# Kernel optimization log

Hardware: AMD Instinct MI355X
Metric: run time of the kernel (lower is better)

## Reference

```python
import jax, jax.numpy as jnp
import numpy as np

B, N, CS, CZ, H, C, PQ, PV = 1, 512, 384, 128, 12, 16, 4, 8
INF, EPS = 1e5, 1e-8


def _quat_to_rot(q):
    # q: [..., 4] unit quaternion -> [..., 3, 3] rotation matrix
    w, x, y, z = q[..., 0], q[..., 1], q[..., 2], q[..., 3]
    r0 = jnp.stack([1 - 2 * (y * y + z * z), 2 * (x * y - w * z), 2 * (x * z + w * y)], -1)
    r1 = jnp.stack([2 * (x * y + w * z), 1 - 2 * (x * x + z * z), 2 * (y * z - w * x)], -1)
    r2 = jnp.stack([2 * (x * z - w * y), 2 * (y * z + w * x), 1 - 2 * (x * x + y * y)], -1)
    return jnp.stack([r0, r1, r2], -2)


def setup_inputs() -> dict:
    key = jax.random.key(0)
    ks = jax.random.split(key, 20)
    sc = 0.02
    quat = jax.random.normal(ks[0], (B, N, 4), jnp.float32)
    quat = quat / jnp.linalg.norm(quat, axis=-1, keepdims=True)
    concat_dim = H * (C + PV * 4 + CZ)
    return {
        "s": jax.random.normal(ks[1], (B, N, CS), jnp.float32),
        "z": jax.random.normal(ks[2], (B, N, N, CZ), jnp.float32),
        "rot": _quat_to_rot(quat),
        "trans": jax.random.normal(ks[3], (B, N, 3), jnp.float32),
        "mask": jnp.ones((B, N), jnp.float32),
        "W_q": jax.random.normal(ks[4], (CS, H * C), jnp.float32) * sc,
        "b_q": jnp.zeros((H * C,), jnp.float32),
        "W_kv": jax.random.normal(ks[5], (CS, 2 * H * C), jnp.float32) * sc,
        "b_kv": jnp.zeros((2 * H * C,), jnp.float32),
        "W_qp": jax.random.normal(ks[6], (CS, H * PQ * 3), jnp.float32) * sc,
        "b_qp": jnp.zeros((H * PQ * 3,), jnp.float32),
        "W_kvp": jax.random.normal(ks[7], (CS, H * (PQ + PV) * 3), jnp.float32) * sc,
        "b_kvp": jnp.zeros((H * (PQ + PV) * 3,), jnp.float32),
        "W_b": jax.random.normal(ks[8], (CZ, H), jnp.float32) * sc,
        "b_b": jnp.zeros((H,), jnp.float32),
        "head_weights": jnp.full((H,), 0.541324854612918, jnp.float32),  # softplus^-1(1)
        "W_out": jax.random.normal(ks[9], (concat_dim, CS), jnp.float32) * sc,
        "b_out": jnp.zeros((CS,), jnp.float32),
    }


def reference(s, z, rot, trans, mask, W_q, b_q, W_kv, b_kv, W_qp, b_qp, W_kvp, b_kvp,
              W_b, b_b, head_weights, W_out, b_out):
    # scalar projections
    q = (s @ W_q + b_q).reshape(*s.shape[:-1], H, C)              # [B,N,H,C]
    kv = (s @ W_kv + b_kv).reshape(*s.shape[:-1], H, 2 * C)
    k, v = kv[..., :C], kv[..., C:]                               # [B,N,H,C]

    def to_global_pts(lin, npts):
        # lin: [B,N,H*npts*3]; torch layout: split into thirds -> stack as xyz
        p = jnp.stack(jnp.split(lin, 3, axis=-1), axis=-1)        # [B,N,H*npts,3]
        g = jnp.einsum('bnij,bnpj->bnpi', rot, p) + trans[:, :, None, :]
        return g.reshape(*g.shape[:-2], H, npts, 3)

    q_pts = to_global_pts(s @ W_qp + b_qp, PQ)                    # [B,N,H,PQ,3]
    kv_pts = to_global_pts(s @ W_kvp + b_kvp, PQ + PV)
    k_pts, v_pts = kv_pts[..., :PQ, :], kv_pts[..., PQ:, :]       # [B,N,H,PQ/PV,3]

    # attention logits
    bias = z @ W_b + b_b                                          # [B,N,N,H]
    a = jnp.einsum('bihc,bjhc->bhij', q, k) * np.sqrt(1.0 / (3 * C))
    a = a + np.sqrt(1.0 / 3.0) * jnp.transpose(bias, (0, 3, 1, 2))

    d = q_pts[:, :, None] - k_pts[:, None]                        # [B,N,N,H,PQ,3]
    pt_att = jnp.sum(d * d, axis=-1)                              # [B,N,N,H,PQ]
    hw = jax.nn.softplus(head_weights) * np.sqrt(1.0 / (3 * (PQ * 9.0 / 2)))
    pt_att = jnp.sum(pt_att * hw[None, None, None, :, None], axis=-1) * (-0.5)  # [B,N,N,H]
    a = a + jnp.transpose(pt_att, (0, 3, 1, 2))

    sq_mask = INF * (mask[:, :, None] * mask[:, None, :] - 1.0)   # [B,N,N]
    a = jax.nn.softmax(a + sq_mask[:, None], axis=-1)             # [B,H,N,N]

    # aggregation
    o = jnp.einsum('bhij,bjhc->bihc', a, v).reshape(*s.shape[:-1], H * C)
    o_pt = jnp.einsum('bhij,bjhpc->bihpc', a, v_pts)              # [B,N,H,PV,3]
    o_pt = jnp.einsum('bnji,bnhpj->bnhpi', rot, o_pt - trans[:, :, None, None, :])
    o_pt_norm = jnp.sqrt(jnp.sum(o_pt ** 2, -1) + EPS).reshape(*s.shape[:-1], H * PV)
    o_pt = o_pt.reshape(*s.shape[:-1], H * PV, 3)
    o_pair = jnp.einsum('bhij,bijc->bihc', a, z).reshape(*s.shape[:-1], H * CZ)

    cat = jnp.concatenate([o, o_pt[..., 0], o_pt[..., 1], o_pt[..., 2], o_pt_norm, o_pair], -1)
    return cat @ W_out + b_out                                    # [B,N,CS]
```

## Files before the change

### kernel.cpp

```cpp
#include <hip/hip_runtime.h>
#include <hip/hip_bf16.h>
#include <math.h>


#define N_    512
#define CS_   384
#define CZ_   128
#define H_    12
#define INF_  100000.0f
#define EPS_  1e-8f

__global__ __launch_bounds__(256) void proj_gemm(
    const float* __restrict__ A,
    const float* __restrict__ W0, const float* __restrict__ b0, float* __restrict__ C0, int N0,
    const float* __restrict__ W1, const float* __restrict__ b1, float* __restrict__ C1, int N1,
    const float* __restrict__ W2, const float* __restrict__ b2, float* __restrict__ C2, int N2,
    const float* __restrict__ W3, const float* __restrict__ b3, float* __restrict__ C3, int N3)
{
    const float* W; const float* bias; float* C; int Nt;
    switch (blockIdx.z) {
        case 0:  W = W0; bias = b0; C = C0; Nt = N0; break;
        case 1:  W = W1; bias = b1; C = C1; Nt = N1; break;
        case 2:  W = W2; bias = b2; C = C2; Nt = N2; break;
        default: W = W3; bias = b3; C = C3; Nt = N3; break;
    }
    const int n0 = blockIdx.y * 64;
    if (n0 >= Nt) return;
    const int m0 = blockIdx.x * 64;

    __shared__ float As[16 * 68];
    __shared__ float Bs[16 * 68];
    const int t  = threadIdx.x;
    const int tm = t & 15;
    const int tn = t >> 4;

    float acc[4][4];
    #pragma unroll
    for (int r = 0; r < 4; ++r)
        #pragma unroll
        for (int c = 0; c < 4; ++c) acc[r][c] = 0.f;

    for (int k0 = 0; k0 < CS_; k0 += 16) {
        {
            int m = t >> 2, kb = (t & 3) * 4;
            float4 a4 = *(const float4*)(A + (size_t)(m0 + m) * CS_ + k0 + kb);
            As[(kb + 0) * 68 + m] = a4.x;
            As[(kb + 1) * 68 + m] = a4.y;
            As[(kb + 2) * 68 + m] = a4.z;
            As[(kb + 3) * 68 + m] = a4.w;
        }
        {
            int kk = t >> 4, n = (t & 15) * 4;
            int gn = n0 + n;
            const float* wr = W + (size_t)(k0 + kk) * Nt;
            float4 b4;
            b4.x = (gn + 0 < Nt) ? wr[gn + 0] : 0.f;
            b4.y = (gn + 1 < Nt) ? wr[gn + 1] : 0.f;
            b4.z = (gn + 2 < Nt) ? wr[gn + 2] : 0.f;
            b4.w = (gn + 3 < Nt) ? wr[gn + 3] : 0.f;
            *(float4*)(Bs + kk * 68 + n) = b4;
        }
        __syncthreads();
        #pragma unroll
        for (int kk = 0; kk < 16; ++kk) {
            float4 a4 = *(const float4*)(As + kk * 68 + tm * 4);
            float4 b4 = *(const float4*)(Bs + kk * 68 + tn * 4);
            float am[4] = {a4.x, a4.y, a4.z, a4.w};
            float bn[4] = {b4.x, b4.y, b4.z, b4.w};
            #pragma unroll
            for (int r = 0; r < 4; ++r)
                #pragma unroll
                for (int c = 0; c < 4; ++c)
                    acc[r][c] = fmaf(am[r], bn[c], acc[r][c]);
        }
        __syncthreads();
    }
    #pragma unroll
    for (int r = 0; r < 4; ++r) {
        int gm = m0 + tm * 4 + r;
        int gn = n0 + tn * 4;
        float* cr = C + (size_t)gm * Nt;
        #pragma unroll
        for (int c = 0; c < 4; ++c)
            if (gn + c < Nt) cr[gn + c] = acc[r][c] + bias[gn + c];
    }
}

__global__ __launch_bounds__(256) void gemm_ksplit(
    const float* __restrict__ A, const float* __restrict__ W,
    float* __restrict__ P)
{
    const int kc = blockIdx.z;
    const int m0 = blockIdx.x * 64;
    const int n0 = blockIdx.y * 64;

    __shared__ float As[16 * 68];
    __shared__ float Bs[16 * 68];
    const int t  = threadIdx.x;
    const int tm = t & 15;
    const int tn = t >> 4;

    float acc[4][4];
    #pragma unroll
    for (int r = 0; r < 4; ++r)
        #pragma unroll
        for (int c = 0; c < 4; ++c) acc[r][c] = 0.f;

    const int kbeg = kc * 192;
    for (int k0 = kbeg; k0 < kbeg + 192; k0 += 16) {
        {
            int m = t >> 2, kb = (t & 3) * 4;
            float4 a4 = *(const float4*)(A + (size_t)(m0 + m) * 2112 + k0 + kb);
            As[(kb + 0) * 68 + m] = a4.x;
            As[(kb + 1) * 68 + m] = a4.y;
            As[(kb + 2) * 68 + m] = a4.z;
            As[(kb + 3) * 68 + m] = a4.w;
        }
        {
            int kk = t >> 4, n = (t & 15) * 4;
            float4 b4 = *(const float4*)(W + (size_t)(k0 + kk) * 384 + n0 + n);
            *(float4*)(Bs + kk * 68 + n) = b4;
        }
        __syncthreads();
        #pragma unroll
        for (int kk = 0; kk < 16; ++kk) {
            float4 a4 = *(const float4*)(As + kk * 68 + tm * 4);
            float4 b4 = *(const float4*)(Bs + kk * 68 + tn * 4);
            float am[4] = {a4.x, a4.y, a4.z, a4.w};
            float bn[4] = {b4.x, b4.y, b4.z, b4.w};
            #pragma unroll
            for (int r = 0; r < 4; ++r)
                #pragma unroll
                for (int c = 0; c < 4; ++c)
                    acc[r][c] = fmaf(am[r], bn[c], acc[r][c]);
        }
        __syncthreads();
    }
    float* Pk = P + (size_t)kc * (512 * 384);
    #pragma unroll
    for (int r = 0; r < 4; ++r) {
        int gm = m0 + tm * 4 + r;
        *(float4*)(Pk + (size_t)gm * 384 + n0 + tn * 4) =
            make_float4(acc[r][0], acc[r][1], acc[r][2], acc[r][3]);
    }
}

__global__ __launch_bounds__(256) void reduce_out(
    const float* __restrict__ P, const float* __restrict__ bias,
    float* __restrict__ out)
{
    int idx = blockIdx.x * 256 + threadIdx.x;
    const float4* b4 = (const float4*)bias;
    float4 s = b4[idx % 96];
    const float4* P4 = (const float4*)P;
    #pragma unroll
    for (int g = 0; g < 11; ++g) {
        float4 v = P4[(size_t)g * 49152 + idx];
        s.x += v.x; s.y += v.y; s.z += v.z; s.w += v.w;
    }
    ((float4*)out)[idx] = s;
}

__global__ __launch_bounds__(192) void prep_points(
    const float* __restrict__ lqp, const float* __restrict__ lkvp,
    const float* __restrict__ rot, const float* __restrict__ trans,
    const float* __restrict__ kvb,
    float* __restrict__ qp, float* __restrict__ kp,
    float* __restrict__ vcat)
{
    const int n = blockIdx.x;
    const int t = threadIdx.x;
    const float* R = rot   + n * 9;
    const float* T = trans + n * 3;

    if (t < 48) {
        float p0 = lqp[n * 144 + t];
        float p1 = lqp[n * 144 + 48 + t];
        float p2 = lqp[n * 144 + 96 + t];
        float* d = qp + n * 144 + t * 3;
        d[0] = R[0]*p0 + R[1]*p1 + R[2]*p2 + T[0];
        d[1] = R[3]*p0 + R[4]*p1 + R[5]*p2 + T[1];
        d[2] = R[6]*p0 + R[7]*p1 + R[8]*p2 + T[2];
    } else {
        int jj = t - 48;
        float p0 = lkvp[n * 432 + jj];
        float p1 = lkvp[n * 432 + 144 + jj];
        float p2 = lkvp[n * 432 + 288 + jj];
        float g0 = R[0]*p0 + R[1]*p1 + R[2]*p2 + T[0];
        float g1 = R[3]*p0 + R[4]*p1 + R[5]*p2 + T[1];
        float g2 = R[6]*p0 + R[7]*p1 + R[8]*p2 + T[2];
        int h = jj / 12, idx = jj % 12;
        if (idx < 4) {
            float* d = kp + n * 144 + (h * 4 + idx) * 3;
            d[0] = g0; d[1] = g1; d[2] = g2;
        } else {
            float* d = vcat + (size_t)n * 512 + 192 + h * 24 + (idx - 4) * 3;
            d[0] = g0; d[1] = g1; d[2] = g2;
        }
    }
    vcat[(size_t)n * 512 + t] = kvb[(size_t)n * 384 + (t >> 4) * 32 + 16 + (t & 15)];
}

__global__ __launch_bounds__(256) void ipa_core(
    const float* __restrict__ z,   const float* __restrict__ q,
    const float* __restrict__ kvb, const float* __restrict__ qp,
    const float* __restrict__ kp,  const float* __restrict__ vcat,
    const float* __restrict__ Wb,  const float* __restrict__ bb,
    const float* __restrict__ hwraw, const float* __restrict__ mask,
    const float* __restrict__ rot, const float* __restrict__ trans,
    float* __restrict__ cat)
{
    __shared__ float4 a_s4[1548];
    __shared__ float4 pb4[2112];
    float* a_s = (float*)a_s4;
    float* pb  = (float*)pb4;

    const int i    = blockIdx.x;
    const int t    = threadIdx.x;
    const int lane = t & 63;

    const float sc_qk = 0.14433756729740643f;
    const float sc_b  = 0.5773502691896258f;
    const float sc_hw = 0.13608276348795434f;

    const float mi = mask[i];

    const int h0 = __builtin_amdgcn_readfirstlane((t >> 6) * 3);
    const float bbA = bb[h0],     bbB = bb[h0 + 1],     bbC = bb[h0 + 2];
    float xA = hwraw[h0], xB = hwraw[h0 + 1], xC = hwraw[h0 + 2];
    const float hwA = ((xA > 20.f) ? xA : log1pf(__expf(xA))) * sc_hw;
    const float hwB = ((xB > 20.f) ? xB : log1pf(__expf(xB))) * sc_hw;
    const float hwC = ((xC > 20.f) ? xC : log1pf(__expf(xC))) * sc_hw;

    const float4* qv  = (const float4*)(q  + (size_t)i * 192);
    const float4* qpv = (const float4*)(qp + (size_t)i * 144);

    float* ztile = pb;
    for (int tile = 0; tile < 8; ++tile) {
        const int jb = tile * 64;
        const float4* zsrc = (const float4*)z + ((size_t)i * N_ + jb) * 32;
        #pragma unroll
        for (int k2 = 0; k2 < 8; ++k2) {
            int idx = t + k2 * 256;
            int rr = idx >> 5, c4 = idx & 31;
            *(float4*)(ztile + rr * 132 + c4 * 4) = zsrc[(size_t)rr * 32 + c4];
        }
        __syncthreads();

        const int j = jb + lane;
        float b0 = bbA, b1 = bbB, b2 = bbC;
        const float4* zrow = (const float4*)(ztile + lane * 132);
        #pragma unroll 8
        for (int c4 = 0; c4 < 32; ++c4) {
            float4 z4 = zrow[c4];
            float zc[4] = {z4.x, z4.y, z4.z, z4.w};
            #pragma unroll
            for (int cc = 0; cc < 4; ++cc) {
                const int c = c4 * 4 + cc;
                b0 = fmaf(zc[cc], Wb[c * 12 + h0    ], b0);
                b1 = fmaf(zc[cc], Wb[c * 12 + h0 + 1], b1);
                b2 = fmaf(zc[cc], Wb[c * 12 + h0 + 2], b2);
            }
        }

        const float mt = INF_ * (mi * mask[j] - 1.f);
        const float4* kr  = (const float4*)(kvb + (size_t)j * 384);
        const float4* kpr = (const float4*)(kp  + (size_t)j * 144);
        #pragma unroll
        for (int hh = 0; hh < 3; ++hh) {
            const int h = h0 + hh;
            float qk = 0.f;
            #pragma unroll
            for (int c4 = 0; c4 < 4; ++c4) {
                float4 qh = qv[h * 4 + c4];
                float4 kh = kr[h * 8 + c4];
                qk = fmaf(qh.x, kh.x, qk);
                qk = fmaf(qh.y, kh.y, qk);
                qk = fmaf(qh.z, kh.z, qk);
                qk = fmaf(qh.w, kh.w, qk);
            }
            float pt = 0.f;
            #pragma unroll
            for (int r = 0; r < 3; ++r) {
                float4 qh = qpv[h * 3 + r];
                float4 kh = kpr[h * 3 + r];
                float d0 = qh.x - kh.x, d1 = qh.y - kh.y;
                float d2 = qh.z - kh.z, d3 = qh.w - kh.w;
                pt = fmaf(d0, d0, pt); pt = fmaf(d1, d1, pt);
                pt = fmaf(d2, d2, pt); pt = fmaf(d3, d3, pt);
            }
            float bsum = (hh == 0) ? b0 : (hh == 1) ? b1 : b2;
            float hwv  = (hh == 0) ? hwA : (hh == 1) ? hwB : hwC;
            a_s[h * 516 + j] = fmaf(qk, sc_qk,
                               fmaf(bsum, sc_b,
                               fmaf(-0.5f * hwv, pt, mt)));
        }
        __syncthreads();
    }

    {
        const int w = t >> 6;
        #pragma unroll
        for (int hh = 0; hh < 3; ++hh) {
            const int h = w + hh * 4;
            float* row = a_s + h * 516;
            float4 v0 = *(float4*)(row + lane * 8);
            float4 v1 = *(float4*)(row + lane * 8 + 4);
            float m = fmaxf(fmaxf(fmaxf(v0.x, v0.y), fmaxf(v0.z, v0.w)),
                            fmaxf(fmaxf(v1.x, v1.y), fmaxf(v1.z, v1.w)));
            #pragma unroll
            for (int off = 32; off > 0; off >>= 1)
                m = fmaxf(m, __shfl_xor(m, off));
            v0.x = __expf(v0.x - m); v0.y = __expf(v0.y - m);
            v0.z = __expf(v0.z - m); v0.w = __expf(v0.w - m);
            v1.x = __expf(v1.x - m); v1.y = __expf(v1.y - m);
            v1.z = __expf(v1.z - m); v1.w = __expf(v1.w - m);
            float s = v0.x + v0.y + v0.z + v0.w + v1.x + v1.y + v1.z + v1.w;
            #pragma unroll
            for (int off = 32; off > 0; off >>= 1)
                s += __shfl_xor(s, off);
            float inv = 1.f / s;
            v0.x *= inv; v0.y *= inv; v0.z *= inv; v0.w *= inv;
            v1.x *= inv; v1.y *= inv; v1.z *= inv; v1.w *= inv;
            *(float4*)(row + lane * 8)     = v0;
            *(float4*)(row + lane * 8 + 4) = v1;
        }
    }
    __syncthreads();

    float* opt_s = pb;
    if (t < 240) {
        const int o0 = 2 * t;
        const int h  = (o0 < 192) ? (o0 >> 4) : ((o0 - 192) / 24);
        const float2* vrow = (const float2*)vcat + t;
        float accx = 0.f, accy = 0.f;
        #pragma unroll 4
        for (int j = 0; j < 512; ++j) {
            float2 v2 = vrow[(size_t)j * 256];
            float aj  = a_s[h * 516 + j];
            accx = fmaf(aj, v2.x, accx);
            accy = fmaf(aj, v2.y, accy);
        }
        if (o0 < 192) {
            cat[(size_t)i * 2112 + o0]     = accx;
            cat[(size_t)i * 2112 + o0 + 1] = accy;
        } else {
            opt_s[o0 - 192] = accx;
            opt_s[o0 - 191] = accy;
        }
    }
    __syncthreads();

    if (t < 96) {
        const float* R = rot   + i * 9;
        const float* T = trans + i * 3;
        float g0 = opt_s[t * 3 + 0] - T[0];
        float g1 = opt_s[t * 3 + 1] - T[1];
        float g2 = opt_s[t * 3 + 2] - T[2];
        float x  = R[0]*g0 + R[3]*g1 + R[6]*g2;
        float y  = R[1]*g0 + R[4]*g1 + R[7]*g2;
        float zz = R[2]*g0 + R[5]*g1 + R[8]*g2;
        float nrm = sqrtf(x*x + y*y + zz*zz + EPS_);
        float* cr = cat + (size_t)i * 2112;
        cr[192 + t] = x;
        cr[288 + t] = y;
        cr[384 + t] = zz;
        cr[480 + t] = nrm;
    }
    __syncthreads();

    {
        const int c4 = t & 31;
        const int jg = t >> 5;
        float4 acc[12];
        #pragma unroll
        for (int h = 0; h < 12; ++h) acc[h] = make_float4(0.f, 0.f, 0.f, 0.f);

        const float4* zr = (const float4*)z + (size_t)i * (N_ * 32) + c4;
        for (int j4b = 0; j4b < 16; ++j4b) {
            const int jb = jg * 64 + j4b * 4;
            float4 zv[4];
            #pragma unroll
            for (int u = 0; u < 4; ++u) zv[u] = zr[(size_t)(jb + u) * 32];
            #pragma unroll
            for (int h = 0; h < 12; ++h) {
                float4 a4 = *(const float4*)(a_s + h * 516 + jb);
                acc[h].x = fmaf(a4.x, zv[0].x, acc[h].x);
                acc[h].y = fmaf(a4.x, zv[0].y, acc[h].y);
                acc[h].z = fmaf(a4.x, zv[0].z, acc[h].z);
                acc[h].w = fmaf(a4.x, zv[0].w, acc[h].w);
                acc[h].x = fmaf(a4.y, zv[1].x, acc[h].x);
                acc[h].y = fmaf(a4.y, zv[1].y, acc[h].y);
                acc[h].z = fmaf(a4.y, zv[1].z, acc[h].z);
                acc[h].w = fmaf(a4.y, zv[1].w, acc[h].w);
                acc[h].x = fmaf(a4.z, zv[2].x, acc[h].x);
                acc[h].y = fmaf(a4.z, zv[2].y, acc[h].y);
                acc[h].z = fmaf(a4.z, zv[2].z, acc[h].z);
                acc[h].w = fmaf(a4.z, zv[2].w, acc[h].w);
                acc[h].x = fmaf(a4.w, zv[3].x, acc[h].x);
                acc[h].y = fmaf(a4.w, zv[3].y, acc[h].y);
                acc[h].z = fmaf(a4.w, zv[3].z, acc[h].z);
                acc[h].w = fmaf(a4.w, zv[3].w, acc[h].w);
            }
        }

        #pragma unroll
        for (int half = 0; half < 2; ++half) {
            __syncthreads();
            #pragma unroll
            for (int hh = 0; hh < 6; ++hh)
                *(float4*)(pb + (size_t)(jg * 6 + hh) * 132 + c4 * 4) = acc[half * 6 + hh];
            __syncthreads();
            #pragma unroll
            for (int k = 0; k < 3; ++k) {
                const int idx = t + k * 256;
                const int hh = idx >> 7, c = idx & 127;
                float s = 0.f;
                #pragma unroll
                for (int g = 0; g < 8; ++g)
                    s += pb[(size_t)(g * 6 + hh) * 132 + c];
                cat[(size_t)i * 2112 + 576 + half * 768 + idx] = s;
            }
        }
    }
}

extern "C" void kernel_launch(void* const* d_in, const int* in_sizes, int n_in,
                              void* d_out, int out_size, void* d_ws, size_t ws_size,
                              hipStream_t stream)
{
    const float* s     = (const float*)d_in[0];
    const float* z     = (const float*)d_in[1];
    const float* rot   = (const float*)d_in[2];
    const float* trans = (const float*)d_in[3];
    const float* mask  = (const float*)d_in[4];
    const float* W_q   = (const float*)d_in[5];
    const float* b_q   = (const float*)d_in[6];
    const float* W_kv  = (const float*)d_in[7];
    const float* b_kv  = (const float*)d_in[8];
    const float* W_qp  = (const float*)d_in[9];
    const float* b_qp  = (const float*)d_in[10];
    const float* W_kvp = (const float*)d_in[11];
    const float* b_kvp = (const float*)d_in[12];
    const float* W_b   = (const float*)d_in[13];
    const float* b_b   = (const float*)d_in[14];
    const float* hw    = (const float*)d_in[15];
    const float* W_out = (const float*)d_in[16];
    const float* b_out = (const float*)d_in[17];
    float* out = (float*)d_out;
    float* ws  = (float*)d_ws;

    float* gpart = ws;
    float* cat   = ws + 2162688;
    float* q     = ws;
    float* kvb   = q    + 98304;
    float* lqp   = kvb  + 196608;
    float* lkvp  = lqp  + 73728;
    float* qp    = lkvp + 221184;
    float* kp    = qp   + 73728;
    float* vcat  = kp   + 73728;

    proj_gemm<<<dim3(8, 7, 4), 256, 0, stream>>>(
        s,
        W_q,   b_q,   q,    192,
        W_kv,  b_kv,  kvb,  384,
        W_qp,  b_qp,  lqp,  144,
        W_kvp, b_kvp, lkvp, 432);
    prep_points<<<512, 192, 0, stream>>>(lqp, lkvp, rot, trans, kvb, qp, kp, vcat);
    ipa_core<<<512, 256, 0, stream>>>(z, q, kvb, qp, kp, vcat,
                                      W_b, b_b, hw, mask, rot, trans, cat);
    gemm_ksplit<<<dim3(8, 6, 11), 256, 0, stream>>>(cat, W_out, gpart);
    reduce_out<<<192, 256, 0, stream>>>(gpart, b_out, out);
}
```

Measured before the change: 387.5 us.

## Split monolithic IPA kernel into GEMM-based logits, bias, softmax and pair-aggregation kernels

The single per-row ipa_core kernel becomes four kernels. qkpt_gemm expands the point-distance term algebraically (|q|^2 + |k|^2 - 2q·k) so the QK and point logits become one tiled GEMM over a concatenated 28-wide feature. logits_k adds the pair bias from z, smax_av does softmax and value aggregation, and opair_k does the z-weighted pair aggregation. The goal is more parallelism and tiled reuse than one 512-block kernel gives. The cost is materialising a 12x512x512 attention tensor in global memory and reading z twice across kernels.

Result: faster. 374.2 us (-3.4%).

```diff
diff --git a/kernel.cpp b/kernel.cpp
--- a/kernel.cpp
+++ b/kernel.cpp
@@ -5,10 +5,16 @@
 
 #define N_    512
 #define CS_   384
-#define CZ_   128
-#define H_    12
 #define INF_  100000.0f
 #define EPS_  1e-8f
+
+#define SC_QK 0.14433756729740643f
+#define SC_B  0.5773502691896258f
+#define SC_HW 0.13608276348795434f
+
+__device__ __forceinline__ float softplus_(float x) {
+    return (x > 20.f) ? x : log1pf(__expf(x));
+}
 
 __global__ __launch_bounds__(256) void proj_gemm(
     const float* __restrict__ A,
@@ -86,87 +92,14 @@
     }
 }
 
-__global__ __launch_bounds__(256) void gemm_ksplit(
-    const float* __restrict__ A, const float* __restrict__ W,
-    float* __restrict__ P)
-{
-    const int kc = blockIdx.z;
-    const int m0 = blockIdx.x * 64;
-    const int n0 = blockIdx.y * 64;
-
-    __shared__ float As[16 * 68];
-    __shared__ float Bs[16 * 68];
-    const int t  = threadIdx.x;
-    const int tm = t & 15;
-    const int tn = t >> 4;
-
-    float acc[4][4];
-    #pragma unroll
-    for (int r = 0; r < 4; ++r)
-        #pragma unroll
-        for (int c = 0; c < 4; ++c) acc[r][c] = 0.f;
-
-    const int kbeg = kc * 192;
-    for (int k0 = kbeg; k0 < kbeg + 192; k0 += 16) {
-        {
-            int m = t >> 2, kb = (t & 3) * 4;
-            float4 a4 = *(const float4*)(A + (size_t)(m0 + m) * 2112 + k0 + kb);
-            As[(kb + 0) * 68 + m] = a4.x;
-            As[(kb + 1) * 68 + m] = a4.y;
-            As[(kb + 2) * 68 + m] = a4.z;
-            As[(kb + 3) * 68 + m] = a4.w;
-        }
-        {
-            int kk = t >> 4, n = (t & 15) * 4;
-            float4 b4 = *(const float4*)(W + (size_t)(k0 + kk) * 384 + n0 + n);
-            *(float4*)(Bs + kk * 68 + n) = b4;
-        }
-        __syncthreads();
-        #pragma unroll
-        for (int kk = 0; kk < 16; ++kk) {
-            float4 a4 = *(const float4*)(As + kk * 68 + tm * 4);
-            float4 b4 = *(const float4*)(Bs + kk * 68 + tn * 4);
-            float am[4] = {a4.x, a4.y, a4.z, a4.w};
-            float bn[4] = {b4.x, b4.y, b4.z, b4.w};
-            #pragma unroll
-            for (int r = 0; r < 4; ++r)
-                #pragma unroll
-                for (int c = 0; c < 4; ++c)
-                    acc[r][c] = fmaf(am[r], bn[c], acc[r][c]);
-        }
-        __syncthreads();
-    }
-    float* Pk = P + (size_t)kc * (512 * 384);
-    #pragma unroll
-    for (int r = 0; r < 4; ++r) {
-        int gm = m0 + tm * 4 + r;
-        *(float4*)(Pk + (size_t)gm * 384 + n0 + tn * 4) =
-            make_float4(acc[r][0], acc[r][1], acc[r][2], acc[r][3]);
-    }
-}
-
-__global__ __launch_bounds__(256) void reduce_out(
-    const float* __restrict__ P, const float* __restrict__ bias,
-    float* __restrict__ out)
-{
-    int idx = blockIdx.x * 256 + threadIdx.x;
-    const float4* b4 = (const float4*)bias;
-    float4 s = b4[idx % 96];
-    const float4* P4 = (const float4*)P;
-    #pragma unroll
-    for (int g = 0; g < 11; ++g) {
-        float4 v = P4[(size_t)g * 49152 + idx];
-        s.x += v.x; s.y += v.y; s.z += v.z; s.w += v.w;
-    }
-    ((float4*)out)[idx] = s;
-}
-
 __global__ __launch_bounds__(192) void prep_points(
     const float* __restrict__ lqp, const float* __restrict__ lkvp,
     const float* __restrict__ rot, const float* __restrict__ trans,
-    const float* __restrict__ kvb,
+    const float* __restrict__ kvb, const float* __restrict__ q,
+    const float* __restrict__ hwraw,
     float* __restrict__ qp, float* __restrict__ kp,
-    float* __restrict__ vcat)
+    float* __restrict__ vcat, float* __restrict__ qcat,
+    float* __restrict__ kcat, float* __restrict__ qn, float* __restrict__ kn)
 {
     const int n = blockIdx.x;
     const int t = threadIdx.x;
@@ -199,110 +132,169 @@
         }
     }
     vcat[(size_t)n * 512 + t] = kvb[(size_t)n * 384 + (t >> 4) * 32 + 16 + (t & 15)];
-}
-
-__global__ __launch_bounds__(256) void ipa_core(
-    const float* __restrict__ z,   const float* __restrict__ q,
-    const float* __restrict__ kvb, const float* __restrict__ qp,
-    const float* __restrict__ kp,  const float* __restrict__ vcat,
-    const float* __restrict__ Wb,  const float* __restrict__ bb,
-    const float* __restrict__ hwraw, const float* __restrict__ mask,
+    __syncthreads();
+
+    {
+        int h = t >> 4, c = t & 15;
+        qcat[((size_t)h * 512 + n) * 28 + c] = q[(size_t)n * 192 + t];
+        kcat[((size_t)h * 512 + n) * 28 + c] = kvb[(size_t)n * 384 + h * 32 + c] * SC_QK;
+    }
+    if (t < 144) {
+        int h = t / 12;
+        float hw = softplus_(hwraw[h]) * SC_HW;
+        qcat[((size_t)h * 512 + n) * 28 + 16 + (t - h * 12)] = qp[n * 144 + t];
+        kcat[((size_t)h * 512 + n) * 28 + 16 + (t - h * 12)] = kp[n * 144 + t] * hw;
+    }
+    if (t < 24) {
+        int h = t % 12;
+        float hw = softplus_(hwraw[h]) * SC_HW;
+        const float* src = (t < 12) ? (qp + n * 144 + h * 12) : (kp + n * 144 + h * 12);
+        float s = 0.f;
+        #pragma unroll
+        for (int r = 0; r < 12; ++r) { float v = src[r]; s = fmaf(v, v, s); }
+        float* dst = (t < 12) ? qn : kn;
+        dst[h * 512 + n] = 0.5f * hw * s;
+    }
+}
+
+__global__ __launch_bounds__(256) void qkpt_gemm(
+    const float* __restrict__ qcat, const float* __restrict__ kcat,
+    const float* __restrict__ qn,   const float* __restrict__ kn,
+    const float* __restrict__ mask, float* __restrict__ att)
+{
+    const int jt = blockIdx.x, it = blockIdx.y, h = blockIdx.z;
+    __shared__ float As[28 * 68];
+    __shared__ float Bs[28 * 68];
+    __shared__ float qn_s[64], kn_s[64], mI[64], mJ[64];
+
+    const int t  = threadIdx.x;
+    const int tm = t & 15;
+    const int tn = t >> 4;
+
+    const float* Aq = qcat + ((size_t)h * 512 + it * 64) * 28;
+    const float* Bk = kcat + ((size_t)h * 512 + jt * 64) * 28;
+    for (int idx = t; idx < 448; idx += 256) {
+        int row = idx / 7, c4 = idx % 7;
+        float4 a4 = *(const float4*)(Aq + row * 28 + c4 * 4);
+        As[(c4 * 4 + 0) * 68 + row] = a4.x;
+        As[(c4 * 4 + 1) * 68 + row] = a4.y;
+        As[(c4 * 4 + 2) * 68 + row] = a4.z;
+        As[(c4 * 4 + 3) * 68 + row] = a4.w;
+        float4 b4 = *(const float4*)(Bk + row * 28 + c4 * 4);
+        Bs[(c4 * 4 + 0) * 68 + row] = b4.x;
+        Bs[(c4 * 4 + 1) * 68 + row] = b4.y;
+        Bs[(c4 * 4 + 2) * 68 + row] = b4.z;
+        Bs[(c4 * 4 + 3) * 68 + row] = b4.w;
+    }
+    if (t < 64) {
+        qn_s[t] = qn[h * 512 + it * 64 + t];
+        mI[t]   = mask[it * 64 + t];
+    } else if (t < 128) {
+        kn_s[t - 64] = kn[h * 512 + jt * 64 + (t - 64)];
+        mJ[t - 64]   = mask[jt * 64 + (t - 64)];
+    }
+    __syncthreads();
+
+    float acc[4][4];
+    #pragma unroll
+    for (int r = 0; r < 4; ++r)
+        #pragma unroll
+        for (int c = 0; c < 4; ++c) acc[r][c] = 0.f;
+
+    #pragma unroll
+    for (int kk = 0; kk < 28; ++kk) {
+        float4 a4 = *(const float4*)(As + kk * 68 + tm * 4);
+        float4 b4 = *(const float4*)(Bs + kk * 68 + tn * 4);
+        float am[4] = {a4.x, a4.y, a4.z, a4.w};
+        float bn[4] = {b4.x, b4.y, b4.z, b4.w};
+        #pragma unroll
+        for (int r = 0; r < 4; ++r)
+            #pragma unroll
+            for (int c = 0; c < 4; ++c)
+                acc[r][c] = fmaf(am[r], bn[c], acc[r][c]);
+    }
+
+    #pragma unroll
+    for (int r = 0; r < 4; ++r) {
+        const int i_ = it * 64 + tm * 4 + r;
+        float* dst = att + ((size_t)h * 512 + i_) * 512 + jt * 64 + tn * 4;
+        float4 o;
+        float qnr = qn_s[tm * 4 + r], mir = mI[tm * 4 + r];
+        o.x = acc[r][0] - qnr - kn_s[tn*4+0] + INF_ * (mir * mJ[tn*4+0] - 1.f);
+        o.y = acc[r][1] - qnr - kn_s[tn*4+1] + INF_ * (mir * mJ[tn*4+1] - 1.f);
+        o.z = acc[r][2] - qnr - kn_s[tn*4+2] + INF_ * (mir * mJ[tn*4+2] - 1.f);
+        o.w = acc[r][3] - qnr - kn_s[tn*4+3] + INF_ * (mir * mJ[tn*4+3] - 1.f);
+        *(float4*)dst = o;
+    }
+}
+
+__global__ __launch_bounds__(256) void logits_k(
+    const float* __restrict__ z, const float* __restrict__ Wb,
+    const float* __restrict__ bb, float* __restrict__ att)
+{
+    __shared__ float ztile[64 * 132];
+    const int jt   = blockIdx.x;
+    const int i    = blockIdx.y;
+    const int jb   = jt * 64;
+    const int t    = threadIdx.x;
+    const int lane = t & 63;
+
+    const int h0 = __builtin_amdgcn_readfirstlane((t >> 6) * 3);
+    const float bbA = bb[h0], bbB = bb[h0 + 1], bbC = bb[h0 + 2];
+
+    const float4* zsrc = (const float4*)z + ((size_t)i * N_ + jb) * 32;
+    #pragma unroll
+    for (int k2 = 0; k2 < 8; ++k2) {
+        int idx = t + k2 * 256;
+        int rr = idx >> 5, c4 = idx & 31;
+        *(float4*)(ztile + rr * 132 + c4 * 4) = zsrc[(size_t)rr * 32 + c4];
+    }
+    __syncthreads();
+
+    float b0 = bbA, b1 = bbB, b2 = bbC;
+    const float4* zrow = (const float4*)(ztile + lane * 132);
+    #pragma unroll 8
+    for (int c4 = 0; c4 < 32; ++c4) {
+        float4 z4 = zrow[c4];
+        float zc[4] = {z4.x, z4.y, z4.z, z4.w};
+        #pragma unroll
+        for (int cc = 0; cc < 4; ++cc) {
+            const int c = c4 * 4 + cc;
+            b0 = fmaf(zc[cc], Wb[c * 12 + h0    ], b0);
+            b1 = fmaf(zc[cc], Wb[c * 12 + h0 + 1], b1);
+            b2 = fmaf(zc[cc], Wb[c * 12 + h0 + 2], b2);
+        }
+    }
+
+    const size_t base = ((size_t)h0 * 512 + i) * 512 + jb + lane;
+    att[base]              = fmaf(SC_B, b0, att[base]);
+    att[base + 262144]     = fmaf(SC_B, b1, att[base + 262144]);
+    att[base + 2 * 262144] = fmaf(SC_B, b2, att[base + 2 * 262144]);
+}
+
+__global__ __launch_bounds__(384) void smax_av(
+    float* __restrict__ att, const float* __restrict__ vcat,
     const float* __restrict__ rot, const float* __restrict__ trans,
     float* __restrict__ cat)
 {
-    __shared__ float4 a_s4[1548];
-    __shared__ float4 pb4[2112];
-    float* a_s = (float*)a_s4;
-    float* pb  = (float*)pb4;
-
+    __shared__ float a_s[12 * 516];
+    __shared__ float opt_s[288];
     const int i    = blockIdx.x;
     const int t    = threadIdx.x;
     const int lane = t & 63;
 
-    const float sc_qk = 0.14433756729740643f;
-    const float sc_b  = 0.5773502691896258f;
-    const float sc_hw = 0.13608276348795434f;
-
-    const float mi = mask[i];
-
-    const int h0 = __builtin_amdgcn_readfirstlane((t >> 6) * 3);
-    const float bbA = bb[h0],     bbB = bb[h0 + 1],     bbC = bb[h0 + 2];
-    float xA = hwraw[h0], xB = hwraw[h0 + 1], xC = hwraw[h0 + 2];
-    const float hwA = ((xA > 20.f) ? xA : log1pf(__expf(xA))) * sc_hw;
-    const float hwB = ((xB > 20.f) ? xB : log1pf(__expf(xB))) * sc_hw;
-    const float hwC = ((xC > 20.f) ? xC : log1pf(__expf(xC))) * sc_hw;
-
-    const float4* qv  = (const float4*)(q  + (size_t)i * 192);
-    const float4* qpv = (const float4*)(qp + (size_t)i * 144);
-
-    float* ztile = pb;
-    for (int tile = 0; tile < 8; ++tile) {
-        const int jb = tile * 64;
-        const float4* zsrc = (const float4*)z + ((size_t)i * N_ + jb) * 32;
-        #pragma unroll
-        for (int k2 = 0; k2 < 8; ++k2) {
-            int idx = t + k2 * 256;
-            int rr = idx >> 5, c4 = idx & 31;
-            *(float4*)(ztile + rr * 132 + c4 * 4) = zsrc[(size_t)rr * 32 + c4];
-        }
-        __syncthreads();
-
-        const int j = jb + lane;
-        float b0 = bbA, b1 = bbB, b2 = bbC;
-        const float4* zrow = (const float4*)(ztile + lane * 132);
-        #pragma unroll 8
-        for (int c4 = 0; c4 < 32; ++c4) {
-            float4 z4 = zrow[c4];
-            float zc[4] = {z4.x, z4.y, z4.z, z4.w};
-            #pragma unroll
-            for (int cc = 0; cc < 4; ++cc) {
-                const int c = c4 * 4 + cc;
-                b0 = fmaf(zc[cc], Wb[c * 12 + h0    ], b0);
-                b1 = fmaf(zc[cc], Wb[c * 12 + h0 + 1], b1);
-                b2 = fmaf(zc[cc], Wb[c * 12 + h0 + 2], b2);
-            }
-        }
-
-        const float mt = INF_ * (mi * mask[j] - 1.f);
-        const float4* kr  = (const float4*)(kvb + (size_t)j * 384);
-        const float4* kpr = (const float4*)(kp  + (size_t)j * 144);
-        #pragma unroll
-        for (int hh = 0; hh < 3; ++hh) {
-            const int h = h0 + hh;
-            float qk = 0.f;
-            #pragma unroll
-            for (int c4 = 0; c4 < 4; ++c4) {
-                float4 qh = qv[h * 4 + c4];
-                float4 kh = kr[h * 8 + c4];
-                qk = fmaf(qh.x, kh.x, qk);
-                qk = fmaf(qh.y, kh.y, qk);
-                qk = fmaf(qh.z, kh.z, qk);
-                qk = fmaf(qh.w, kh.w, qk);
-            }
-            float pt = 0.f;
-            #pragma unroll
-            for (int r = 0; r < 3; ++r) {
-                float4 qh = qpv[h * 3 + r];
-                float4 kh = kpr[h * 3 + r];
-                float d0 = qh.x - kh.x, d1 = qh.y - kh.y;
-                float d2 = qh.z - kh.z, d3 = qh.w - kh.w;
-                pt = fmaf(d0, d0, pt); pt = fmaf(d1, d1, pt);
-                pt = fmaf(d2, d2, pt); pt = fmaf(d3, d3, pt);
-            }
-            float bsum = (hh == 0) ? b0 : (hh == 1) ? b1 : b2;
-            float hwv  = (hh == 0) ? hwA : (hh == 1) ? hwB : hwC;
-            a_s[h * 516 + j] = fmaf(qk, sc_qk,
-                               fmaf(bsum, sc_b,
-                               fmaf(-0.5f * hwv, pt, mt)));
-        }
-        __syncthreads();
-    }
+    for (int idx = t; idx < 1536; idx += 384) {
+        int h = idx >> 7, j4 = idx & 127;
+        *(float4*)(a_s + h * 516 + j4 * 4) =
+            *((const float4*)att + ((size_t)h * 512 + i) * 128 + j4);
+    }
+    __syncthreads();
 
     {
         const int w = t >> 6;
         #pragma unroll
-        for (int hh = 0; hh < 3; ++hh) {
-            const int h = w + hh * 4;
+        for (int hh = 0; hh < 2; ++hh) {
+            const int h = w * 2 + hh;
             float* row = a_s + h * 516;
             float4 v0 = *(float4*)(row + lane * 8);
             float4 v1 = *(float4*)(row + lane * 8 + 4);
@@ -328,13 +320,18 @@
     }
     __syncthreads();
 
-    float* opt_s = pb;
+    for (int idx = t; idx < 1536; idx += 384) {
+        int h = idx >> 7, j4 = idx & 127;
+        *((float4*)att + ((size_t)h * 512 + i) * 128 + j4) =
+            *(const float4*)(a_s + h * 516 + j4 * 4);
+    }
+
     if (t < 240) {
         const int o0 = 2 * t;
         const int h  = (o0 < 192) ? (o0 >> 4) : ((o0 - 192) / 24);
         const float2* vrow = (const float2*)vcat + t;
         float accx = 0.f, accy = 0.f;
-        #pragma unroll 4
+        #pragma unroll 8
         for (int j = 0; j < 512; ++j) {
             float2 v2 = vrow[(size_t)j * 256];
             float aj  = a_s[h * 516 + j];
@@ -367,62 +364,146 @@
         cr[384 + t] = zz;
         cr[480 + t] = nrm;
     }
-    __syncthreads();
-
-    {
-        const int c4 = t & 31;
-        const int jg = t >> 5;
-        float4 acc[12];
-        #pragma unroll
-        for (int h = 0; h < 12; ++h) acc[h] = make_float4(0.f, 0.f, 0.f, 0.f);
-
-        const float4* zr = (const float4*)z + (size_t)i * (N_ * 32) + c4;
-        for (int j4b = 0; j4b < 16; ++j4b) {
-            const int jb = jg * 64 + j4b * 4;
-            float4 zv[4];
-            #pragma unroll
-            for (int u = 0; u < 4; ++u) zv[u] = zr[(size_t)(jb + u) * 32];
-            #pragma unroll
-            for (int h = 0; h < 12; ++h) {
-                float4 a4 = *(const float4*)(a_s + h * 516 + jb);
-                acc[h].x = fmaf(a4.x, zv[0].x, acc[h].x);
-                acc[h].y = fmaf(a4.x, zv[0].y, acc[h].y);
-                acc[h].z = fmaf(a4.x, zv[0].z, acc[h].z);
-                acc[h].w = fmaf(a4.x, zv[0].w, acc[h].w);
-                acc[h].x = fmaf(a4.y, zv[1].x, acc[h].x);
-                acc[h].y = fmaf(a4.y, zv[1].y, acc[h].y);
-                acc[h].z = fmaf(a4.y, zv[1].z, acc[h].z);
-                acc[h].w = fmaf(a4.y, zv[1].w, acc[h].w);
-                acc[h].x = fmaf(a4.z, zv[2].x, acc[h].x);
-                acc[h].y = fmaf(a4.z, zv[2].y, acc[h].y);
-                acc[h].z = fmaf(a4.z, zv[2].z, acc[h].z);
-                acc[h].w = fmaf(a4.z, zv[2].w, acc[h].w);
-                acc[h].x = fmaf(a4.w, zv[3].x, acc[h].x);
-                acc[h].y = fmaf(a4.w, zv[3].y, acc[h].y);
-                acc[h].z = fmaf(a4.w, zv[3].z, acc[h].z);
-                acc[h].w = fmaf(a4.w, zv[3].w, acc[h].w);
-            }
-        }
-
-        #pragma unroll
-        for (int half = 0; half < 2; ++half) {
-            __syncthreads();
-            #pragma unroll
-            for (int hh = 0; hh < 6; ++hh)
-                *(float4*)(pb + (size_t)(jg * 6 + hh) * 132 + c4 * 4) = acc[half * 6 + hh];
-            __syncthreads();
-            #pragma unroll
-            for (int k = 0; k < 3; ++k) {
-                const int idx = t + k * 256;
+}
+
+__global__ __launch_bounds__(512) void opair_k(
+    const float* __restrict__ att, const float* __restrict__ z,
+    float* __restrict__ cat)
+{
+    __shared__ float pb[16 * 6 * 132];
+    const int i  = blockIdx.x;
+    const int t  = threadIdx.x;
+    const int c4 = t & 31;
+    const int jg = t >> 5;
+
+    float4 acc[12];
+    #pragma unroll
+    for (int h = 0; h < 12; ++h) acc[h] = make_float4(0.f, 0.f, 0.f, 0.f);
+
+    const float4* zr = (const float4*)z + (size_t)i * (N_ * 32) + c4;
+    #pragma unroll 2
+    for (int j4b = 0; j4b < 8; ++j4b) {
+        const int jb = jg * 32 + j4b * 4;
+        float4 zv[4];
+        #pragma unroll
+        for (int u = 0; u < 4; ++u) zv[u] = zr[(size_t)(jb + u) * 32];
+        #pragma unroll
+        for (int h = 0; h < 12; ++h) {
+            float4 a4 = *(const float4*)(att + ((size_t)h * 512 + i) * 512 + jb);
+            acc[h].x = fmaf(a4.x, zv[0].x, acc[h].x);
+            acc[h].y = fmaf(a4.x, zv[0].y, acc[h].y);
+            acc[h].z = fmaf(a4.x, zv[0].z, acc[h].z);
+            acc[h].w = fmaf(a4.x, zv[0].w, acc[h].w);
+            acc[h].x = fmaf(a4.y, zv[1].x, acc[h].x);
+            acc[h].y = fmaf(a4.y, zv[1].y, acc[h].y);
+            acc[h].z = fmaf(a4.y, zv[1].z, acc[h].z);
+            acc[h].w = fmaf(a4.y, zv[1].w, acc[h].w);
+            acc[h].x = fmaf(a4.z, zv[2].x, acc[h].x);
+            acc[h].y = fmaf(a4.z, zv[2].y, acc[h].y);
+            acc[h].z = fmaf(a4.z, zv[2].z, acc[h].z);
+            acc[h].w = fmaf(a4.z, zv[2].w, acc[h].w);
+            acc[h].x = fmaf(a4.w, zv[3].x, acc[h].x);
+            acc[h].y = fmaf(a4.w, zv[3].y, acc[h].y);
+            acc[h].z = fmaf(a4.w, zv[3].z, acc[h].z);
+            acc[h].w = fmaf(a4.w, zv[3].w, acc[h].w);
+        }
+    }
+
+    #pragma unroll
+    for (int half = 0; half < 2; ++half) {
+        __syncthreads();
+        #pragma unroll
+        for (int hh = 0; hh < 6; ++hh)
+            *(float4*)(pb + (size_t)(jg * 6 + hh) * 132 + c4 * 4) = acc[half * 6 + hh];
+        __syncthreads();
+        #pragma unroll
+        for (int k = 0; k < 2; ++k) {
+            const int idx = t + k * 512;
+            if (idx < 768) {
                 const int hh = idx >> 7, c = idx & 127;
                 float s = 0.f;
                 #pragma unroll
-                for (int g = 0; g < 8; ++g)
+                for (int g = 0; g < 16; ++g)
                     s += pb[(size_t)(g * 6 + hh) * 132 + c];
                 cat[(size_t)i * 2112 + 576 + half * 768 + idx] = s;
             }
         }
     }
+}
+
+__global__ __launch_bounds__(256) void gemm_ksplit(
+    const float* __restrict__ A, const float* __restrict__ W,
+    float* __restrict__ P)
+{
+    const int kc = blockIdx.z;
+    const int m0 = blockIdx.x * 64;
+    const int n0 = blockIdx.y * 64;
+
+    __shared__ float As[16 * 68];
+    __shared__ float Bs[16 * 68];
+    const int t  = threadIdx.x;
+    const int tm = t & 15;
+    const int tn = t >> 4;
+
+    float acc[4][4];
+    #pragma unroll
+    for (int r = 0; r < 4; ++r)
+        #pragma unroll
+        for (int c = 0; c < 4; ++c) acc[r][c] = 0.f;
+
+    const int kbeg = kc * 192;
+    for (int k0 = kbeg; k0 < kbeg + 192; k0 += 16) {
+        {
+            int m = t >> 2, kb = (t & 3) * 4;
+            float4 a4 = *(const float4*)(A + (size_t)(m0 + m) * 2112 + k0 + kb);
+            As[(kb + 0) * 68 + m] = a4.x;
+            As[(kb + 1) * 68 + m] = a4.y;
+            As[(kb + 2) * 68 + m] = a4.z;
+            As[(kb + 3) * 68 + m] = a4.w;
+        }
+        {
+            int kk = t >> 4, n = (t & 15) * 4;
+            float4 b4 = *(const float4*)(W + (size_t)(k0 + kk) * 384 + n0 + n);
+            *(float4*)(Bs + kk * 68 + n) = b4;
+        }
+        __syncthreads();
+        #pragma unroll
+        for (int kk = 0; kk < 16; ++kk) {
+            float4 a4 = *(const float4*)(As + kk * 68 + tm * 4);
+            float4 b4 = *(const float4*)(Bs + kk * 68 + tn * 4);
+            float am[4] = {a4.x, a4.y, a4.z, a4.w};
+            float bn[4] = {b4.x, b4.y, b4.z, b4.w};
+            #pragma unroll
+            for (int r = 0; r < 4; ++r)
+                #pragma unroll
+                for (int c = 0; c < 4; ++c)
+                    acc[r][c] = fmaf(am[r], bn[c], acc[r][c]);
+        }
+        __syncthreads();
+    }
+    float* Pk = P + (size_t)kc * (512 * 384);
+    #pragma unroll
+    for (int r = 0; r < 4; ++r) {
+        int gm = m0 + tm * 4 + r;
+        *(float4*)(Pk + (size_t)gm * 384 + n0 + tn * 4) =
+            make_float4(acc[r][0], acc[r][1], acc[r][2], acc[r][3]);
+    }
+}
+
+__global__ __launch_bounds__(256) void reduce_out(
+    const float* __restrict__ P, const float* __restrict__ bias,
+    float* __restrict__ out)
+{
+    int idx = blockIdx.x * 256 + threadIdx.x;
+    const float4* b4 = (const float4*)bias;
+    float4 s = b4[idx % 96];
+    const float4* P4 = (const float4*)P;
+    #pragma unroll
+    for (int g = 0; g < 11; ++g) {
+        float4 v = P4[(size_t)g * 49152 + idx];
+        s.x += v.x; s.y += v.y; s.z += v.z; s.w += v.w;
+    }
+    ((float4*)out)[idx] = s;
 }
 
 extern "C" void kernel_launch(void* const* d_in, const int* in_sizes, int n_in,
@@ -450,15 +531,20 @@
     float* out = (float*)d_out;
     float* ws  = (float*)d_ws;
 
-    float* gpart = ws;
-    float* cat   = ws + 2162688;
-    float* q     = ws;
-    float* kvb   = q    + 98304;
-    float* lqp   = kvb  + 196608;
-    float* lkvp  = lqp  + 73728;
-    float* qp    = lkvp + 221184;
-    float* kp    = qp   + 73728;
-    float* vcat  = kp   + 73728;
+    float* att   = ws;
+    float* cat   = att   + 3145728;
+    float* q     = cat   + 1081344;
+    float* kvb   = q     + 98304;
+    float* lqp   = kvb   + 196608;
+    float* lkvp  = lqp   + 73728;
+    float* qp    = lkvp  + 221184;
+    float* kp    = qp    + 73728;
+    float* vcat  = kp    + 73728;
+    float* qcat  = vcat  + 262144;
+    float* kcat  = qcat  + 172032;
+    float* qn    = kcat  + 172032;
+    float* kn    = qn    + 6144;
+    float* gpart = kn    + 6144;
 
     proj_gemm<<<dim3(8, 7, 4), 256, 0, stream>>>(
         s,
@@ -466,9 +552,12 @@
         W_kv,  b_kv,  kvb,  384,
         W_qp,  b_qp,  lqp,  144,
         W_kvp, b_kvp, lkvp, 432);
-    prep_points<<<512, 192, 0, stream>>>(lqp, lkvp, rot, trans, kvb, qp, kp, vcat);
-    ipa_core<<<512, 256, 0, stream>>>(z, q, kvb, qp, kp, vcat,
-                                      W_b, b_b, hw, mask, rot, trans, cat);
+    prep_points<<<512, 192, 0, stream>>>(lqp, lkvp, rot, trans, kvb, q, hw,
+                                         qp, kp, vcat, qcat, kcat, qn, kn);
+    qkpt_gemm<<<dim3(8, 8, 12), 256, 0, stream>>>(qcat, kcat, qn, kn, mask, att);
+    logits_k<<<dim3(8, 512), 256, 0, stream>>>(z, W_b, b_b, att);
+    smax_av<<<512, 384, 0, stream>>>(att, vcat, rot, trans, cat);
+    opair_k<<<512, 512, 0, stream>>>(att, z, cat);
     gemm_ksplit<<<dim3(8, 6, 11), 256, 0, stream>>>(cat, W_out, gpart);
     reduce_out<<<192, 256, 0, stream>>>(gpart, b_out, out);
 }
```
